# Performance work log

Measured on AMD Instinct MI355X. Metric: run time of the kernel, lower is better.

Reference implementation:

```python
import jax, jax.numpy as jnp
import numpy as np

LEVEL_NUM = 8  # init kwarg level_num (scale is unused by forward)


def setup_inputs() -> dict:
    key = jax.random.key(0)
    x = jax.random.normal(key, (1, 1024, 1024), dtype=jnp.float32)
    return {"x": x}


def reference(x):
    N, H, W = x.shape
    L = LEVEL_NUM
    q_levels = jnp.linspace(x.min(), x.max(), L)          # (L,)
    sigma = 2.0 / L                                        # 1 / (level_num/2)
    # soft quantization: (N,H,W,L)
    quant = jnp.exp(-((x[..., None] - q_levels) ** 2) / (sigma ** 2))
    quant = jnp.transpose(quant, (0, 3, 1, 2))             # (N,L,H,W)
    quant = jnp.pad(quant, ((0, 0), (0, 0), (0, 1), (0, 1)))  # (N,L,H+1,W+1)
    quant_left = quant[:, :, None, :H, :W]                 # (N,L,1,H,W)
    quant_right = quant[:, None, :, 1:, 1:]                # (N,1,L,H,W)
    co_occurrence = quant_left * quant_right               # (N,L,L,H,W)
    sta = co_occurrence.sum(axis=(-1, -2))                 # (N,L,L)
    sta = sta / sta.sum(axis=(1, 2))                       # valid since N==1
    # q_levels_h[n,i,j] = q_levels[j]; q_levels_w[n,i,j] = q_levels[i]
    q_h = jnp.broadcast_to(q_levels[None, None, :], (N, L, L))
    q_w = jnp.broadcast_to(q_levels[None, :, None], (N, L, L))
    output = jnp.stack([q_h, q_w, sta], axis=1).reshape(N, 3, L * L)[0]  # (3, L*L)
    return output, quant[0], co_occurrence[0]
```

## Files before the change

kernel.cpp:

```cpp
#include <hip/hip_runtime.h>

#define H 1024
#define W 1024
#define L 8
#define QH 1025
#define QW 1025
#define OUT0 192
#define QUANT_ELEMS (L * QH * QW)

#define UROWS 16
#define NUNITS 512

#define WS_MINP 0
#define WS_MAXP 256
#define WS_STA  512

__device__ __forceinline__ float qlev(float mn, float step, float mx, int i) {
    return (i == L - 1) ? mx : mn + step * (float)i;
}
__device__ __forceinline__ float ex16(float x, float q) {
    float d = x - q;
    return __expf(-16.f * d * d);
}

__global__ __launch_bounds__(256) void k_minmax(const float4* __restrict__ x4,
                                                float* __restrict__ ws) {
    const int t = threadIdx.x, b = blockIdx.x;
    float mn = 1e30f, mx = -1e30f;
    #pragma unroll
    for (int i = 0; i < 4; ++i) {
        float4 v = x4[b * 1024 + i * 256 + t];
        mn = fminf(mn, fminf(fminf(v.x, v.y), fminf(v.z, v.w)));
        mx = fmaxf(mx, fmaxf(fmaxf(v.x, v.y), fmaxf(v.z, v.w)));
    }
    #pragma unroll
    for (int m = 1; m < 64; m <<= 1) {
        mn = fminf(mn, __shfl_xor(mn, m, 64));
        mx = fmaxf(mx, __shfl_xor(mx, m, 64));
    }
    __shared__ float smn[4], smx[4];
    if ((t & 63) == 0) { smn[t >> 6] = mn; smx[t >> 6] = mx; }
    __syncthreads();
    if (t == 0) {
        ws[WS_MINP + b] = fminf(fminf(smn[0], smn[1]), fminf(smn[2], smn[3]));
        ws[WS_MAXP + b] = fmaxf(fmaxf(smx[0], smx[1]), fmaxf(smx[2], smx[3]));
    }
}

__global__ __launch_bounds__(256) void k_main(const float* __restrict__ x,
                                              float* __restrict__ out,
                                              float* __restrict__ ws) {
    const int t = threadIdx.x;
    __shared__ float smn[4], smx[4];
    __shared__ float red[4][8];

    float mn = ws[WS_MINP + t], mx = ws[WS_MAXP + t];
    #pragma unroll
    for (int m = 1; m < 64; m <<= 1) {
        mn = fminf(mn, __shfl_xor(mn, m, 64));
        mx = fmaxf(mx, __shfl_xor(mx, m, 64));
    }
    if ((t & 63) == 0) { smn[t >> 6] = mn; smx[t >> 6] = mx; }
    __syncthreads();
    const float mnv = fminf(fminf(smn[0], smn[1]), fminf(smn[2], smn[3]));
    const float mxv = fmaxf(fmaxf(smx[0], smx[1]), fmaxf(smx[2], smx[3]));
    const float step = (mxv - mnv) * (1.0f / 7.0f);
    float qv[L];
    #pragma unroll
    for (int j = 0; j < L; ++j) qv[j] = qlev(mnv, step, mxv, j);

    float* __restrict__ quant = out + OUT0;
    float* __restrict__ co    = out + OUT0 + QUANT_ELEMS;

    const int sbid = (blockIdx.x & 7) * (NUNITS / 8) + (blockIdx.x >> 3);
    const int c = sbid >> 4, i = (sbid >> 1) & 7, half = sbid & 1;
    const int r0 = c * 32 + half * UROWS;
    const float qi = qv[i];

    const int w0 = t * 4;
    const bool ok3 = (w0 + 4 < W);

    float4 cur = *(const float4*)(x + r0 * W + w0);
    float4 nxt = make_float4(0.f, 0.f, 0.f, 0.f);
    float e = 0.f;
    if (r0 + 1 < H) {
        nxt = *(const float4*)(x + (r0 + 1) * W + w0);
        if (ok3) e = x[(r0 + 1) * W + w0 + 4];
    }

    float acc[L] = {0.f, 0.f, 0.f, 0.f, 0.f, 0.f, 0.f, 0.f};

    for (int r = 0; r < UROWS; ++r) {
        const int h = r0 + r;
        float4 nx2 = make_float4(0.f, 0.f, 0.f, 0.f);
        float e2 = 0.f;
        if (h + 2 < H) {
            nx2 = *(const float4*)(x + (h + 2) * W + w0);
            if (ok3) e2 = x[(h + 2) * W + w0 + 4];
        }

        float l0 = ex16(cur.x, qi), l1 = ex16(cur.y, qi),
              l2 = ex16(cur.z, qi), l3 = ex16(cur.w, qi);
        float* qp = quant + (i * QH + h) * QW + w0;
        *(float4*)qp = make_float4(l0, l1, l2, l3);
        if (t == 255) qp[4] = 0.0f;

        float* cb = co + (i * L) * (H * W) + h * W + w0;
        if (h + 1 < H) {
            #pragma unroll
            for (int j = 0; j < L; ++j) {
                const float q = qv[j];
                float p0 = ex16(nxt.y, q);
                float p1 = ex16(nxt.z, q);
                float p2 = ex16(nxt.w, q);
                float p3 = ok3 ? ex16(e, q) : 0.f;
                float v0 = l0 * p0, v1 = l1 * p1, v2 = l2 * p2, v3 = l3 * p3;
                *(float4*)(cb + j * (H * W)) = make_float4(v0, v1, v2, v3);
                acc[j] += (v0 + v1) + (v2 + v3);
            }
        } else {
            #pragma unroll
            for (int j = 0; j < L; ++j)
                *(float4*)(cb + j * (H * W)) = make_float4(0.f, 0.f, 0.f, 0.f);
        }

        cur = nxt; nxt = nx2; e = e2;
    }

    if (c == NUNITS / 16 - 1 && half == 1) {
        for (int w = t; w < QW; w += 256)
            quant[(i * QH + H) * QW + w] = 0.0f;
    }

    #pragma unroll
    for (int j = 0; j < L; ++j) {
        float a = acc[j];
        #pragma unroll
        for (int m = 1; m < 64; m <<= 1) a += __shfl_xor(a, m, 64);
        if ((t & 63) == 0) red[t >> 6][j] = a;
    }
    __syncthreads();
    if (t < L) {
        float s = (red[0][t] + red[1][t]) + (red[2][t] + red[3][t]);
        ws[WS_STA + (c * 2 + half) * 64 + i * 8 + t] = s;
    }
}

__global__ void k_final(float* __restrict__ out, const float* __restrict__ ws) {
    const int t = threadIdx.x;
    float mn = 1e30f, mx = -1e30f;
    #pragma unroll
    for (int i = 0; i < 4; ++i) {
        mn = fminf(mn, ws[WS_MINP + i * 64 + t]);
        mx = fmaxf(mx, ws[WS_MAXP + i * 64 + t]);
    }
    #pragma unroll
    for (int m = 1; m < 64; m <<= 1) {
        mn = fminf(mn, __shfl_xor(mn, m, 64));
        mx = fmaxf(mx, __shfl_xor(mx, m, 64));
    }
    const float step = (mx - mn) * (1.0f / 7.0f);

    float s = 0.f;
    #pragma unroll 8
    for (int u = 0; u < 64; ++u) s += ws[WS_STA + u * 64 + t];
    float tot = s;
    #pragma unroll
    for (int m = 1; m < 64; m <<= 1) tot += __shfl_xor(tot, m, 64);

    out[t]       = qlev(mn, step, mx, t & 7);
    out[64 + t]  = qlev(mn, step, mx, t >> 3);
    out[128 + t] = s / tot;
}

extern "C" void kernel_launch(void* const* d_in, const int* in_sizes, int n_in,
                              void* d_out, int out_size, void* d_ws, size_t ws_size,
                              hipStream_t stream) {
    const float* x = (const float*)d_in[0];
    float* out = (float*)d_out;
    float* ws = (float*)d_ws;

    k_minmax<<<dim3(256), dim3(256), 0, stream>>>((const float4*)x, ws);
    k_main<<<dim3(NUNITS), dim3(256), 0, stream>>>(x, out, ws);
    k_final<<<dim3(1), dim3(64), 0, stream>>>(out, ws);
}
```

Measured before the change: 64.70 us.

## Fuse min/max, main, and final kernels into one cooperative kernel with grid syncs

Replaces three separate kernel launches with a single cooperative launch that does the min/max reduction, then grid-syncs, does the quantization and co-occurrence pass, grid-syncs again, and has block 0 write the normalized statistics. This removes two kernel launch boundaries and their gaps. In exchange it adds two grid-wide barriers and requires all 512 blocks to be co-resident, and the cooperative launch path may carry its own overhead.

```diff
diff --git a/kernel.cpp b/kernel.cpp
--- a/kernel.cpp
+++ b/kernel.cpp
@@ -1,4 +1,7 @@
 #include <hip/hip_runtime.h>
+#include <hip/hip_cooperative_groups.h>
+
+namespace cg = cooperative_groups;
 
 #define H 1024
 #define W 1024
@@ -12,8 +15,8 @@
 #define NUNITS 512
 
 #define WS_MINP 0
-#define WS_MAXP 256
-#define WS_STA  512
+#define WS_MAXP 512
+#define WS_STA  1024
 
 __device__ __forceinline__ float qlev(float mn, float step, float mx, int i) {
     return (i == L - 1) ? mx : mn + step * (float)i;
@@ -23,38 +26,39 @@
     return __expf(-16.f * d * d);
 }
 
-__global__ __launch_bounds__(256) void k_minmax(const float4* __restrict__ x4,
-                                                float* __restrict__ ws) {
-    const int t = threadIdx.x, b = blockIdx.x;
-    float mn = 1e30f, mx = -1e30f;
-    #pragma unroll
-    for (int i = 0; i < 4; ++i) {
-        float4 v = x4[b * 1024 + i * 256 + t];
-        mn = fminf(mn, fminf(fminf(v.x, v.y), fminf(v.z, v.w)));
-        mx = fmaxf(mx, fmaxf(fmaxf(v.x, v.y), fmaxf(v.z, v.w)));
-    }
-    #pragma unroll
-    for (int m = 1; m < 64; m <<= 1) {
-        mn = fminf(mn, __shfl_xor(mn, m, 64));
-        mx = fmaxf(mx, __shfl_xor(mx, m, 64));
-    }
-    __shared__ float smn[4], smx[4];
-    if ((t & 63) == 0) { smn[t >> 6] = mn; smx[t >> 6] = mx; }
-    __syncthreads();
-    if (t == 0) {
-        ws[WS_MINP + b] = fminf(fminf(smn[0], smn[1]), fminf(smn[2], smn[3]));
-        ws[WS_MAXP + b] = fmaxf(fmaxf(smx[0], smx[1]), fmaxf(smx[2], smx[3]));
-    }
-}
-
-__global__ __launch_bounds__(256) void k_main(const float* __restrict__ x,
-                                              float* __restrict__ out,
-                                              float* __restrict__ ws) {
+__global__ __launch_bounds__(256) void k_fused(const float* __restrict__ x,
+                                               float* __restrict__ out,
+                                               float* __restrict__ ws) {
+    cg::grid_group grid = cg::this_grid();
     const int t = threadIdx.x;
+    const int bid = blockIdx.x;
     __shared__ float smn[4], smx[4];
     __shared__ float red[4][8];
 
-    float mn = ws[WS_MINP + t], mx = ws[WS_MAXP + t];
+    {
+        const float4* x4 = (const float4*)x;
+        float4 a = x4[bid * 512 + t];
+        float4 b = x4[bid * 512 + 256 + t];
+        float mn = fminf(fminf(fminf(a.x, a.y), fminf(a.z, a.w)),
+                         fminf(fminf(b.x, b.y), fminf(b.z, b.w)));
+        float mx = fmaxf(fmaxf(fmaxf(a.x, a.y), fmaxf(a.z, a.w)),
+                         fmaxf(fmaxf(b.x, b.y), fmaxf(b.z, b.w)));
+        #pragma unroll
+        for (int m = 1; m < 64; m <<= 1) {
+            mn = fminf(mn, __shfl_xor(mn, m, 64));
+            mx = fmaxf(mx, __shfl_xor(mx, m, 64));
+        }
+        if ((t & 63) == 0) { smn[t >> 6] = mn; smx[t >> 6] = mx; }
+        __syncthreads();
+        if (t == 0) {
+            ws[WS_MINP + bid] = fminf(fminf(smn[0], smn[1]), fminf(smn[2], smn[3]));
+            ws[WS_MAXP + bid] = fmaxf(fmaxf(smx[0], smx[1]), fmaxf(smx[2], smx[3]));
+        }
+    }
+    grid.sync();
+
+    float mn = fminf(ws[WS_MINP + t], ws[WS_MINP + 256 + t]);
+    float mx = fmaxf(ws[WS_MAXP + t], ws[WS_MAXP + 256 + t]);
     #pragma unroll
     for (int m = 1; m < 64; m <<= 1) {
         mn = fminf(mn, __shfl_xor(mn, m, 64));
@@ -72,7 +76,7 @@
     float* __restrict__ quant = out + OUT0;
     float* __restrict__ co    = out + OUT0 + QUANT_ELEMS;
 
-    const int sbid = (blockIdx.x & 7) * (NUNITS / 8) + (blockIdx.x >> 3);
+    const int sbid = (bid & 7) * (NUNITS / 8) + (bid >> 3);
     const int c = sbid >> 4, i = (sbid >> 1) & 7, half = sbid & 1;
     const int r0 = c * 32 + half * UROWS;
     const float qi = qv[i];
@@ -144,33 +148,21 @@
         float s = (red[0][t] + red[1][t]) + (red[2][t] + red[3][t]);
         ws[WS_STA + (c * 2 + half) * 64 + i * 8 + t] = s;
     }
-}
 
-__global__ void k_final(float* __restrict__ out, const float* __restrict__ ws) {
-    const int t = threadIdx.x;
-    float mn = 1e30f, mx = -1e30f;
-    #pragma unroll
-    for (int i = 0; i < 4; ++i) {
-        mn = fminf(mn, ws[WS_MINP + i * 64 + t]);
-        mx = fmaxf(mx, ws[WS_MAXP + i * 64 + t]);
+    grid.sync();
+
+    if (bid == 0 && t < 64) {
+        float s = 0.f;
+        #pragma unroll 8
+        for (int u = 0; u < 64; ++u) s += ws[WS_STA + u * 64 + t];
+        float tot = s;
+        #pragma unroll
+        for (int m = 1; m < 64; m <<= 1) tot += __shfl_xor(tot, m, 64);
+
+        out[t]       = qv[t & 7];
+        out[64 + t]  = qv[t >> 3];
+        out[128 + t] = s / tot;
     }
-    #pragma unroll
-    for (int m = 1; m < 64; m <<= 1) {
-        mn = fminf(mn, __shfl_xor(mn, m, 64));
-        mx = fmaxf(mx, __shfl_xor(mx, m, 64));
-    }
-    const float step = (mx - mn) * (1.0f / 7.0f);
-
-    float s = 0.f;
-    #pragma unroll 8
-    for (int u = 0; u < 64; ++u) s += ws[WS_STA + u * 64 + t];
-    float tot = s;
-    #pragma unroll
-    for (int m = 1; m < 64; m <<= 1) tot += __shfl_xor(tot, m, 64);
-
-    out[t]       = qlev(mn, step, mx, t & 7);
-    out[64 + t]  = qlev(mn, step, mx, t >> 3);
-    out[128 + t] = s / tot;
 }
 
 extern "C" void kernel_launch(void* const* d_in, const int* in_sizes, int n_in,
@@ -180,7 +172,7 @@
     float* out = (float*)d_out;
     float* ws = (float*)d_ws;
 
-    k_minmax<<<dim3(256), dim3(256), 0, stream>>>((const float4*)x, ws);
-    k_main<<<dim3(NUNITS), dim3(256), 0, stream>>>(x, out, ws);
-    k_final<<<dim3(1), dim3(64), 0, stream>>>(out, ws);
+    void* args[] = {(void*)&x, (void*)&out, (void*)&ws};
+    hipLaunchCooperativeKernel((const void*)k_fused, dim3(NUNITS), dim3(256),
+                               args, 0, stream);
 }
```

New measurement: 164.8 us. +154.7%, slower.
